# Kernel tuning notes

Hardware: AMD Instinct MI355X
Metric: run time of the kernel (lower is better)

## Reference

```python
import jax, jax.numpy as jnp
import numpy as np

UNITS = 4096                                # number of heap nodes (power of two)
DEPTH = (UNITS - 1).bit_length() + 1        # 13 heap steps (k = 0..12)
FEATURES = [2, 64, 64, 2]
BATCH = 256


def _build_heap_maps(nodes):
    """For each heap step k, precompute for every output node j the input
    (ancestor) node index it reads from, plus a validity mask. This encodes
    exactly the torch block loop: for level l, input nodes [floor(2^(l-1)), 2^l)
    broadcast (repeat_interleave by heap_factor) into output range
    [out_node0, out_node1), with blocks where out_node1 > nodes skipped."""
    depth = (nodes - 1).bit_length() + 1
    maps = []
    for k in range(depth):
        idx = np.zeros(nodes, np.int32)
        mask = np.zeros(nodes, np.bool_)
        for l in range(depth):
            in0 = 0 if l == 0 else 2 ** (l - 1)
            if in0 == 0:  # root block (node 0)
                hf = 1 if k == 0 else 2 ** (k - 1)      # ceil(2^(k-1))
                out0 = 0 if k == 0 else 2 ** (k - 1)    # floor(2^(k-1))
                out1 = out0 + hf
            else:
                hf = 2 ** k
                out0 = in0 * hf
                out1 = (2 ** l) * hf
            if out1 <= nodes:
                js = np.arange(out0, out1)
                idx[js] = in0 + (js - out0) // hf
                mask[js] = True
        maps.append((jnp.asarray(idx), jnp.asarray(mask)))
    return maps


MAPS = _build_heap_maps(UNITS)


def heap_linear(x, W, b, minheap):
    # x: [..., nodes, in_f]; W: [K, out_f, in_f]; b: [K, out_f]; K = DEPTH - minheap
    out = jnp.zeros(x.shape[:-1] + (W.shape[1],), jnp.float32)
    for i, k in enumerate(range(minheap, DEPTH)):
        idx, mask = MAPS[k]
        # apply linear_k to every node once, then gather parent -> children
        y = jnp.einsum('...ni,oi->...no', x, W[i]) + b[i]
        out = out + jnp.where(mask[:, None], y[..., idx, :], 0.0)
    return out


def setup_inputs() -> dict:
    key = jax.random.key(0)
    ks = jax.random.split(key, 7)
    f0, f1, f2, f3 = FEATURES

    def w(k, n, o, i):
        return jax.random.normal(k, (n, o, i), jnp.float32) / np.float32(np.sqrt(i))

    return {
        "x": jax.random.normal(ks[0], (BATCH, UNITS, f0), jnp.float32),
        "W1": w(ks[1], DEPTH - 1, f1, f0),   # minheap=1 -> 12 sublayers
        "b1": jax.random.normal(ks[2], (DEPTH - 1, f1), jnp.float32) * 0.01,
        "W2": w(ks[3], DEPTH, f2, f1),       # minheap=0 -> 13 sublayers
        "b2": jax.random.normal(ks[4], (DEPTH, f2), jnp.float32) * 0.01,
        "W3": w(ks[5], DEPTH, f3, f2),
        "b3": jax.random.normal(ks[6], (DEPTH, f3), jnp.float32) * 0.01,
    }


def reference(x, W1, b1, W2, b2, W3, b3):
    h = heap_linear(x, W1, b1, minheap=1)
    h = jax.nn.relu(h)
    h = heap_linear(h, W2, b2, minheap=0)
    h = jax.nn.relu(h)
    logits = heap_linear(h, W3, b3, minheap=0)
    return logits
```

## Files before the change

### kernel.cpp

```cpp
#include <hip/hip_runtime.h>

#define UNITS 4096
#define DEPTH 13
#define BATCH 256

typedef __attribute__((ext_vector_type(8))) short s16x8;
typedef __attribute__((ext_vector_type(4))) float f32x4;
typedef __attribute__((ext_vector_type(4))) int   i32x4;

__device__ __forceinline__ unsigned short f2bf(float f){
  unsigned u = __builtin_bit_cast(unsigned, f);
  u += 0x7FFFu + ((u >> 16) & 1u);
  return (unsigned short)(u >> 16);
}
__device__ __forceinline__ int levelof(int j){ return j ? (32 - __clz(j)) : 0; }

struct FragA { s16x8 v[2]; };
struct FragB { s16x8 v[2][4]; };

__device__ __forceinline__ void gll16(const void* g, void* l){
  __builtin_amdgcn_global_load_lds(
      (const __attribute__((address_space(1))) unsigned int*)g,
      (__attribute__((address_space(3))) unsigned int*)l, 16, 0, 0);
}

__device__ __forceinline__ void load_afragG(FragA& f, const unsigned short* __restrict__ Hq,
                                            int rowbase, int l15, int kg){
  #pragma unroll
  for (int kk = 0; kk < 2; ++kk)
    f.v[kk] = *(const s16x8*)(Hq + ((size_t)((kk*4 + kg)*256 + rowbase + l15))*8);
}
__device__ __forceinline__ void load_bfragG(FragB& f, const unsigned short* __restrict__ Wf,
                                            int lane){
  #pragma unroll
  for (int kk = 0; kk < 2; ++kk)
    #pragma unroll
    for (int n = 0; n < 4; ++n)
      f.v[kk][n] = *(const s16x8*)(Wf + ((size_t)((kk*4 + n)*64 + lane))*8);
}
__device__ __forceinline__ void ld_afragL(FragA& f, const char* Ab, int wid, int l15, int kg){
  #pragma unroll
  for (int kk = 0; kk < 2; ++kk)
    f.v[kk] = *(const s16x8*)(Ab + (kk*4 + kg)*1024 + (wid*16 + l15)*16);
}
__device__ __forceinline__ void ld_bfragL(FragB& f, const char* Bb, int lane){
  #pragma unroll
  for (int kk = 0; kk < 2; ++kk)
    #pragma unroll
    for (int n = 0; n < 4; ++n)
      f.v[kk][n] = *(const s16x8*)(Bb + ((kk*4 + n)*64 + lane)*16);
}
__device__ __forceinline__ void mstep(f32x4 acc[4], const FragA& A, const FragB& B){
  #pragma unroll
  for (int kk = 0; kk < 2; ++kk)
    #pragma unroll
    for (int n = 0; n < 4; ++n)
      acc[n] = __builtin_amdgcn_mfma_f32_16x16x32_bf16(A.v[kk], B.v[kk][n], acc[n], 0, 0, 0);
}
__device__ __forceinline__ void negA(FragA& A){
  const i32x4 sgn = {(int)0x80008000, (int)0x80008000, (int)0x80008000, (int)0x80008000};
  #pragma unroll
  for (int kk = 0; kk < 2; ++kk){
    i32x4 t = __builtin_bit_cast(i32x4, A.v[kk]);
    t ^= sgn;
    A.v[kk] = __builtin_bit_cast(s16x8, t);
  }
}

__device__ __forceinline__ float rowsum16(float s){
  int v, u;
  v = __builtin_bit_cast(int, s);
  u = __builtin_amdgcn_update_dpp(v, v, 0xB1, 0xF, 0xF, false);
  s += __builtin_bit_cast(float, u);
  v = __builtin_bit_cast(int, s);
  u = __builtin_amdgcn_update_dpp(v, v, 0x4E, 0xF, 0xF, false);
  s += __builtin_bit_cast(float, u);
  v = __builtin_bit_cast(int, s);
  u = __builtin_amdgcn_update_dpp(v, v, 0x141, 0xF, 0xF, false);
  s += __builtin_bit_cast(float, u);
  v = __builtin_bit_cast(int, s);
  u = __builtin_amdgcn_update_dpp(v, v, 0x140, 0xF, 0xF, false);
  s += __builtin_bit_cast(float, u);
  return s;
}

__device__ __forceinline__ void epilogue(const f32x4 acc[4], int p, int lp,
    const float cbv[4], const float* w3s,
    float* __restrict__ y3, int rowbase, int l15, int kg){
  int tmax = 11 - lp;
  for (int tt = 0; tt <= tmax; ++tt){
    float w30[4], w31[4];
    #pragma unroll
    for (int n = 0; n < 4; ++n){
      w30[n] = w3s[(tt*2 + 0)*64 + n*16 + l15];
      w31[n] = w3s[(tt*2 + 1)*64 + n*16 + l15];
    }
    int off = 4096 - (4096 >> tt);
    #pragma unroll
    for (int reg = 0; reg < 4; ++reg){
      float s0 = 0.f, s1 = 0.f;
      #pragma unroll
      for (int n = 0; n < 4; ++n){
        float hv = fmaxf(acc[n][reg] + cbv[n], 0.f);
        s0 = fmaf(w30[n], hv, s0);
        s1 = fmaf(w31[n], hv, s1);
      }
      s0 = rowsum16(s0);
      s1 = rowsum16(s1);
      if (l15 == 0){
        int b = rowbase + kg*4 + reg;
        float2 v; v.x = s0; v.y = s1;
        *(float2*)(y3 + ((size_t)(off + p)*256 + b)*2) = v;
      }
    }
  }
}

__global__ __launch_bounds__(256) void k_prep(const float* __restrict__ W2,
    const float* __restrict__ W1, const float* __restrict__ W3,
    const float* __restrict__ b1, const float* __restrict__ b2, const float* __restrict__ b3,
    unsigned short* __restrict__ W2f, unsigned short* __restrict__ W1f,
    float* __restrict__ cb1, float* __restrict__ cb2, float* __restrict__ cb3,
    float* __restrict__ w3h20){
  int blk = blockIdx.x, t = threadIdx.x;
  if (blk < 26){
    int u = blk*256 + t;
    int lane = u & 63, c = (u >> 6) & 7, k = u >> 9;
    int n = c & 3, kk = c >> 2, l15 = lane & 15, kg = lane >> 4;
    s16x8 rr;
    #pragma unroll
    for (int e = 0; e < 8; ++e)
      rr[e] = (short)f2bf(W2[((size_t)(k*64 + n*16 + l15))*64 + kk*32 + kg*8 + e]);
    *(s16x8*)(W2f + (size_t)u*8) = rr;
  } else if (blk == 26){
    int n = t >> 6, lane = t & 63, l15 = lane & 15, kg = lane >> 4;
    int f = n*16 + l15;
    s16x8 r = {0,0,0,0,0,0,0,0};
    #pragma unroll
    for (int j = 0; j < 4; ++j){
      int m = kg*4 + j;
      if (m < DEPTH-1){
        r[2*j]   = (short)f2bf(W1[(m*64 + f)*2]);
        r[2*j+1] = (short)f2bf(W1[(m*64 + f)*2 + 1]);
      }
    }
    *(s16x8*)(W1f + (size_t)t*8) = r;
  } else {
    if (t < 64){
      float r = 0.f;
      cb1[t] = 0.f;
      for (int m = 1; m < DEPTH; ++m){ r += b1[(m-1)*64 + t]; cb1[m*64 + t] = r; }
      float r2 = 0.f;
      for (int m = 0; m < DEPTH; ++m){ r2 += b2[m*64 + t]; cb2[m*64 + t] = r2; }
    } else if (t < 66){
      int o = t - 64;
      float r = 0.f;
      for (int m = 0; m < DEPTH; ++m){ r += b3[m*2 + o]; cb3[m*2 + o] = r; }
    } else if (t >= 128 && t < 128 + DEPTH*2){
      int q = t - 128, tt = q >> 1, o = q & 1;
      float s = 0.f;
      for (int f = 0; f < 64; ++f)
        s = fmaf(W3[(tt*2 + o)*64 + f], fmaxf(b2[f], 0.f), s);
      w3h20[tt*2 + o] = s;
    }
  }
}

__global__ __launch_bounds__(256) void k_xpose(const float* __restrict__ x,
                                               float* __restrict__ xT){
  __shared__ float2 tile[64][65];
  int jb = (blockIdx.x & 63) * 64;
  int bb = (blockIdx.x >> 6) * 64;
  int t = threadIdx.x;
  #pragma unroll
  for (int i = 0; i < 16; ++i){
    int idx = i*256 + t;
    int jj = idx & 63, b = idx >> 6;
    tile[jj][b] = *(const float2*)(x + (((size_t)(bb + b))*UNITS + jb + jj)*2);
  }
  __syncthreads();
  #pragma unroll
  for (int i = 0; i < 16; ++i){
    int idx = i*256 + t;
    int b = idx & 63, jj = idx >> 6;
    *(float2*)(xT + (((size_t)(jb + jj))*BATCH + bb + b)*2) = tile[jj][b];
  }
}

__global__ __launch_bounds__(256) void k_GH(const float* __restrict__ xT,
    const unsigned short* __restrict__ W1f, const float* __restrict__ cb1,
    unsigned short* __restrict__ H){
  __shared__ unsigned short tile[BATCH*64];
  int p = blockIdx.x;
  int lvl = levelof(p);
  int t = threadIdx.x, wid = t >> 6, lane = t & 63, l15 = lane & 15, kg = lane >> 4;

  s16x8 af[4];
  #pragma unroll
  for (int m = 0; m < 4; ++m){
    int b = wid*64 + m*16 + l15;
    s16x8 r = {0,0,0,0,0,0,0,0};
    #pragma unroll
    for (int j = 0; j < 4; ++j){
      int mm = kg*4 + j;
      if (mm <= lvl){
        float2 xv = *(const float2*)(xT + ((size_t)(p >> mm)*BATCH + b)*2);
        r[2*j]   = (short)f2bf(xv.x);
        r[2*j+1] = (short)f2bf(xv.y);
      }
    }
    af[m] = r;
  }
  f32x4 acc[4][4];
  #pragma unroll
  for (int m = 0; m < 4; ++m)
    #pragma unroll
    for (int n = 0; n < 4; ++n) acc[m][n] = (f32x4){0.f,0.f,0.f,0.f};
  #pragma unroll
  for (int n = 0; n < 4; ++n){
    s16x8 bf = *(const s16x8*)(W1f + ((size_t)n*64 + lane)*8);
    #pragma unroll
    for (int m = 0; m < 4; ++m)
      acc[m][n] = __builtin_amdgcn_mfma_f32_16x16x32_bf16(af[m], bf, acc[m][n], 0, 0, 0);
  }
  int lvl1 = lvl + 1;
  float cbv[4];
  #pragma unroll
  for (int n = 0; n < 4; ++n) cbv[n] = cb1[lvl1*64 + n*16 + l15];
  #pragma unroll
  for (int m = 0; m < 4; ++m)
    #pragma unroll
    for (int n = 0; n < 4; ++n)
      #pragma unroll
      for (int i = 0; i < 4; ++i){
        int row = wid*64 + m*16 + kg*4 + i;
        int col = n*16 + l15;
        float v = fmaxf(acc[m][n][i] + cbv[n], 0.f);
        *(unsigned short*)((char*)tile + ((row*128 + col*2) ^ ((row & 7) << 4))) = f2bf(v);
      }
  __syncthreads();
  #pragma unroll
  for (int i = 0; i < 8; ++i){
    s16x8 v = *(const s16x8*)((const char*)tile + ((t*128 + i*16) ^ ((t & 7) << 4)));
    *(s16x8*)(H + (size_t)p*16384 + ((size_t)i*256 + t)*8) = v;
  }
}

__global__ __launch_bounds__(256, 3) void k_F11(const unsigned short* __restrict__ H,
    const unsigned short* __restrict__ W2f, const float* __restrict__ cb2,
    const float* __restrict__ W3, float* __restrict__ y3){
  __shared__ char As[2*8192];
  __shared__ char Bs[2*8192];
  __shared__ float w3s[26*64];

  int bid = blockIdx.x;
  int slice = bid >> 9;
  int r = bid & 511;
  int q = 511 - ((r & 7)*64 + (r >> 3));
  int t = threadIdx.x, wid = t >> 6, lane = t & 63, l15 = lane & 15, kg = lane >> 4;
  int rowbase = slice*64 + wid*16;

  const char* Hb   = (const char*)H;
  const char* W2fb = (const char*)W2f;

  #pragma unroll
  for (int i = 0; i < 2; ++i){
    int idx = i*256 + t;
    if (idx < 416) ((float4*)w3s)[idx] = ((const float4*)W3)[idx];
  }

  f32x4 acc[4];
  #pragma unroll
  for (int n = 0; n < 4; ++n) acc[n] = (f32x4){0.f, 0.f, 0.f, 0.f};

  if (q == 0){
    __syncthreads();
    FragA A; FragB B;
    for (int p = 0; p < 4; ++p){
      int lp = levelof(p);
      float cbv[4];
      #pragma unroll
      for (int n = 0; n < 4; ++n) cbv[n] = cb2[(lp+1)*64 + n*16 + l15];
      #pragma unroll
      for (int n = 0; n < 4; ++n) acc[n] = (f32x4){0.f, 0.f, 0.f, 0.f};
      for (int k = 0; k <= lp; ++k){
        load_bfragG(B, W2f + (size_t)k*4096, lane);
        load_afragG(A, H + (size_t)(p >> k)*16384, rowbase, l15, kg);
        mstep(acc, A, B);
      }
      epilogue(acc, p, lp, cbv, w3s, y3, rowbase, l15, kg);
    }
    return;
  }

  const int L = levelof(q) + 2;
  const int S = L + 5;
  float cbv[4];
  #pragma unroll
  for (int n = 0; n < 4; ++n) cbv[n] = cb2[(L+1)*64 + n*16 + l15];

  auto stage = [&](int u){
    int tileA; const char* Wk;
    if (u <= L-2){
      tileA = q >> u;
      Wk = W2fb + (size_t)(u+2)*8192;
    } else {
      int d = u - (L-1);
      tileA = (d==0) ? 2*q : (d==1) ? 4*q : (d==2) ? 4*q+1
            : (d==3) ? 2*q+1 : (d==4) ? 4*q+2 : 4*q+3;
      Wk = (d==0 || d==3) ? (W2fb + 8192) : W2fb;
    }
    const char* Ht = Hb + (size_t)tileA*32768;
    char* Ab = As + (u & 1)*8192;
    char* Bb = Bs + (u & 1)*8192;
    #pragma unroll
    for (int j = 0; j < 2; ++j){
      int piece = wid*2 + j;
      gll16(Ht + piece*4096 + (slice*64 + lane)*16, Ab + piece*1024);
    }
    #pragma unroll
    for (int j = 0; j < 2; ++j){
      int c = wid*2 + j;
      gll16(Wk + c*1024 + lane*16, Bb + c*1024);
    }
  };

  stage(0);
  __syncthreads();

  FragA held0, held1;

  for (int s = 0; s < S; ++s){
    if (s + 1 < S) stage(s + 1);
    const char* Ab = As + (s & 1)*8192;
    const char* Bb = Bs + (s & 1)*8192;
    FragB bF; ld_bfragL(bF, Bb, lane);
    if (s <= L-2){
      FragA aF; ld_afragL(aF, Ab, wid, l15, kg);
      mstep(acc, aF, bF);
    } else {
      int d = s - (L-1);
      if (d == 0){
        ld_afragL(held0, Ab, wid, l15, kg);
        mstep(acc, held0, bF);
      } else if (d == 1){
        ld_afragL(held1, Ab, wid, l15, kg);
        mstep(acc, held1, bF);
        epilogue(acc, 4*q, L, cbv, w3s, y3, rowbase, l15, kg);
      } else if (d == 2){
        negA(held1); mstep(acc, held1, bF);
        ld_afragL(held1, Ab, wid, l15, kg);
        mstep(acc, held1, bF);
        epilogue(acc, 4*q + 1, L, cbv, w3s, y3, rowbase, l15, kg);
      } else if (d == 3){
        negA(held0); mstep(acc, held0, bF);
        FragA aF; ld_afragL(aF, Ab, wid, l15, kg);
        mstep(acc, aF, bF);
      } else if (d == 4){
        negA(held1); mstep(acc, held1, bF);
        ld_afragL(held1, Ab, wid, l15, kg);
        mstep(acc, held1, bF);
        epilogue(acc, 4*q + 2, L, cbv, w3s, y3, rowbase, l15, kg);
      } else {
        negA(held1); mstep(acc, held1, bF);
        FragA aF; ld_afragL(aF, Ab, wid, l15, kg);
        mstep(acc, aF, bF);
        epilogue(acc, 4*q + 3, L, cbv, w3s, y3, rowbase, l15, kg);
      }
    }
    __syncthreads();
  }
}

__global__ __launch_bounds__(256) void k_scatter(const float* __restrict__ y3,
    const float* __restrict__ cb3, const float* __restrict__ w3h20,
    float* __restrict__ out){
  int i = blockIdx.x;
  int b = threadIdx.x;
  float4 o[4];
  #pragma unroll
  for (int c = 0; c < 4; ++c){
    int p = i*4 + c;
    int lp = levelof(p);
    float s0 = cb3[(lp+1)*2]     + w3h20[(lp+1)*2];
    float s1 = cb3[(lp+1)*2 + 1] + w3h20[(lp+1)*2 + 1];
    for (int k = 0; k <= lp; ++k){
      int pi = (4096 - (4096 >> k)) + (p >> k);
      float2 v = *(const float2*)(y3 + ((size_t)pi*256 + b)*2);
      s0 += v.x; s1 += v.y;
    }
    if (p == 0){
      o[c].x = cb3[0] + w3h20[0];
      o[c].y = cb3[1] + w3h20[1];
      o[c].z = s0; o[c].w = s1;
    } else {
      o[c].x = s0; o[c].y = s1; o[c].z = s0; o[c].w = s1;
    }
  }
  float4* dst = (float4*)(out + (size_t)b*8192 + (size_t)i*16);
  #pragma unroll
  for (int c = 0; c < 4; ++c) dst[c] = o[c];
}

extern "C" void kernel_launch(void* const* d_in, const int* in_sizes, int n_in,
                              void* d_out, int out_size, void* d_ws, size_t ws_size,
                              hipStream_t stream){
  const float* x  = (const float*)d_in[0];
  const float* W1 = (const float*)d_in[1];
  const float* b1 = (const float*)d_in[2];
  const float* W2 = (const float*)d_in[3];
  const float* b2 = (const float*)d_in[4];
  const float* W3 = (const float*)d_in[5];
  const float* b3 = (const float*)d_in[6];
  float* out = (float*)d_out;
  char* ws = (char*)d_ws;

  unsigned short* W2f   = (unsigned short*)(ws + 0);
  unsigned short* W1f   = (unsigned short*)(ws + 106496);
  float* cb1   = (float*)(ws + 110592);
  float* cb2   = (float*)(ws + 113920);
  float* cb3   = (float*)(ws + 117248);
  float* w3h20 = (float*)(ws + 117376);
  float* xT    = (float*)(ws + 117504);
  unsigned short* H = (unsigned short*)(ws + 8506112);
  float* y3    = (float*)(ws + 75614976);

  hipLaunchKernelGGL(k_prep,    dim3(28),   dim3(256), 0, stream, W2, W1, W3, b1, b2, b3, W2f, W1f, cb1, cb2, cb3, w3h20);
  hipLaunchKernelGGL(k_xpose,   dim3(256),  dim3(256), 0, stream, x, xT);
  hipLaunchKernelGGL(k_GH,      dim3(2048), dim3(256), 0, stream, xT, W1f, cb1, H);
  hipLaunchKernelGGL(k_F11,     dim3(2048), dim3(256), 0, stream, H, W2f, cb2, W3, y3);
  hipLaunchKernelGGL(k_scatter, dim3(512),  dim3(256), 0, stream, y3, cb3, w3h20, out);
}
```

Baseline: 123.4 us.

## Compute layer-3 projection epilogue with MFMA instead of scalar FMA and DPP reductions

The third-layer projection, which applies all 26 W3 rows to the relu'd hidden tile, moves from scalar FMAs plus 16-lane DPP row reductions onto bf16 MFMA instructions. The hidden tile goes through a small per-wave swizzled LDS scratch, and W3 is pre-packed into MFMA fragments in a new prep block. Results are kept in registers and stored together at the end. This cuts VALU and cross-lane work in the epilogue, at the cost of bf16 rounding of the hidden activations, extra LDS traffic and more live registers.

```diff
diff --git a/kernel.cpp b/kernel.cpp
--- a/kernel.cpp
+++ b/kernel.cpp
@@ -67,59 +67,31 @@
   }
 }
 
-__device__ __forceinline__ float rowsum16(float s){
-  int v, u;
-  v = __builtin_bit_cast(int, s);
-  u = __builtin_amdgcn_update_dpp(v, v, 0xB1, 0xF, 0xF, false);
-  s += __builtin_bit_cast(float, u);
-  v = __builtin_bit_cast(int, s);
-  u = __builtin_amdgcn_update_dpp(v, v, 0x4E, 0xF, 0xF, false);
-  s += __builtin_bit_cast(float, u);
-  v = __builtin_bit_cast(int, s);
-  u = __builtin_amdgcn_update_dpp(v, v, 0x141, 0xF, 0xF, false);
-  s += __builtin_bit_cast(float, u);
-  v = __builtin_bit_cast(int, s);
-  u = __builtin_amdgcn_update_dpp(v, v, 0x140, 0xF, 0xF, false);
-  s += __builtin_bit_cast(float, u);
-  return s;
-}
-
-__device__ __forceinline__ void epilogue(const f32x4 acc[4], int p, int lp,
-    const float cbv[4], const float* w3s,
-    float* __restrict__ y3, int rowbase, int l15, int kg){
-  int tmax = 11 - lp;
-  for (int tt = 0; tt <= tmax; ++tt){
-    float w30[4], w31[4];
-    #pragma unroll
-    for (int n = 0; n < 4; ++n){
-      w30[n] = w3s[(tt*2 + 0)*64 + n*16 + l15];
-      w31[n] = w3s[(tt*2 + 1)*64 + n*16 + l15];
-    }
-    int off = 4096 - (4096 >> tt);
+__device__ __forceinline__ void epi_mfma(const f32x4 acc[4], const float cbv[4],
+    char* scr, const s16x8 (&w3a)[2][2], f32x4& d0, f32x4& d1,
+    int l15, int kg){
+  #pragma unroll
+  for (int n = 0; n < 4; ++n)
     #pragma unroll
     for (int reg = 0; reg < 4; ++reg){
-      float s0 = 0.f, s1 = 0.f;
-      #pragma unroll
-      for (int n = 0; n < 4; ++n){
-        float hv = fmaxf(acc[n][reg] + cbv[n], 0.f);
-        s0 = fmaf(w30[n], hv, s0);
-        s1 = fmaf(w31[n], hv, s1);
-      }
-      s0 = rowsum16(s0);
-      s1 = rowsum16(s1);
-      if (l15 == 0){
-        int b = rowbase + kg*4 + reg;
-        float2 v; v.x = s0; v.y = s1;
-        *(float2*)(y3 + ((size_t)(off + p)*256 + b)*2) = v;
-      }
-    }
-  }
+      float hv = fmaxf(acc[n][reg] + cbv[n], 0.f);
+      int a16 = (kg*4 + reg)*64 + ((n*16 + l15) ^ (kg << 4));
+      *(unsigned short*)(scr + a16*2) = f2bf(hv);
+    }
+  int key = (l15 >> 2) << 4;
+  s16x8 b0 = *(const s16x8*)(scr + (size_t)(l15*64 + ((kg*8)      ^ key))*2);
+  s16x8 b1 = *(const s16x8*)(scr + (size_t)(l15*64 + ((32 + kg*8) ^ key))*2);
+  d0 = __builtin_amdgcn_mfma_f32_16x16x32_bf16(w3a[0][0], b0, d0, 0, 0, 0);
+  d0 = __builtin_amdgcn_mfma_f32_16x16x32_bf16(w3a[1][0], b1, d0, 0, 0, 0);
+  d1 = __builtin_amdgcn_mfma_f32_16x16x32_bf16(w3a[0][1], b0, d1, 0, 0, 0);
+  d1 = __builtin_amdgcn_mfma_f32_16x16x32_bf16(w3a[1][1], b1, d1, 0, 0, 0);
 }
 
 __global__ __launch_bounds__(256) void k_prep(const float* __restrict__ W2,
     const float* __restrict__ W1, const float* __restrict__ W3,
     const float* __restrict__ b1, const float* __restrict__ b2, const float* __restrict__ b3,
     unsigned short* __restrict__ W2f, unsigned short* __restrict__ W1f,
+    unsigned short* __restrict__ W3Af,
     float* __restrict__ cb1, float* __restrict__ cb2, float* __restrict__ cb3,
     float* __restrict__ w3h20){
   int blk = blockIdx.x, t = threadIdx.x;
@@ -145,6 +117,17 @@
       }
     }
     *(s16x8*)(W1f + (size_t)t*8) = r;
+  } else if (blk == 27){
+    int lane = t & 63, tile = (t >> 6) & 1, kk = t >> 7;
+    int l15 = lane & 15, kg = lane >> 4;
+    int row = tile*16 + l15;
+    s16x8 r = {0,0,0,0,0,0,0,0};
+    if (row < 26){
+      #pragma unroll
+      for (int e = 0; e < 8; ++e)
+        r[e] = (short)f2bf(W3[(size_t)row*64 + kk*32 + kg*8 + e]);
+    }
+    *(s16x8*)(W3Af + (size_t)t*8) = r;
   } else {
     if (t < 64){
       float r = 0.f;
@@ -246,12 +229,27 @@
   }
 }
 
-__global__ __launch_bounds__(256, 3) void k_F11(const unsigned short* __restrict__ H,
-    const unsigned short* __restrict__ W2f, const float* __restrict__ cb2,
-    const float* __restrict__ W3, float* __restrict__ y3){
+#define STORE_D(dv0, dv1, pp, lpv) { \
+  int cnt = 2*(12 - (lpv)); \
+  _Pragma("unroll") \
+  for (int tile_ = 0; tile_ < 2; ++tile_){ \
+    _Pragma("unroll") \
+    for (int reg_ = 0; reg_ < 4; ++reg_){ \
+      int ttp = tile_*16 + kg*4 + reg_; \
+      if (ttp < cnt){ \
+        int tt = ttp >> 1, o = ttp & 1; \
+        int offp = 4096 - (4096 >> tt); \
+        y3[((size_t)(offp + (pp))*256 + rowbase + l15)*2 + o] = (tile_ ? (dv1)[reg_] : (dv0)[reg_]); \
+      } \
+    } \
+  } }
+
+__global__ __launch_bounds__(256, 3) void k_F12(const unsigned short* __restrict__ H,
+    const unsigned short* __restrict__ W2f, const unsigned short* __restrict__ W3Af,
+    const float* __restrict__ cb2, float* __restrict__ y3){
   __shared__ char As[2*8192];
   __shared__ char Bs[2*8192];
-  __shared__ float w3s[26*64];
+  __shared__ char scr_all[4*2048];
 
   int bid = blockIdx.x;
   int slice = bid >> 9;
@@ -259,37 +257,68 @@
   int q = 511 - ((r & 7)*64 + (r >> 3));
   int t = threadIdx.x, wid = t >> 6, lane = t & 63, l15 = lane & 15, kg = lane >> 4;
   int rowbase = slice*64 + wid*16;
+  char* scr = scr_all + wid*2048;
 
   const char* Hb   = (const char*)H;
   const char* W2fb = (const char*)W2f;
 
-  #pragma unroll
-  for (int i = 0; i < 2; ++i){
-    int idx = i*256 + t;
-    if (idx < 416) ((float4*)w3s)[idx] = ((const float4*)W3)[idx];
-  }
+  s16x8 w3a[2][2];
+  #pragma unroll
+  for (int kk = 0; kk < 2; ++kk)
+    #pragma unroll
+    for (int tile = 0; tile < 2; ++tile)
+      w3a[kk][tile] = *(const s16x8*)(W3Af + ((size_t)((kk*2 + tile)*64 + lane))*8);
 
   f32x4 acc[4];
   #pragma unroll
   for (int n = 0; n < 4; ++n) acc[n] = (f32x4){0.f, 0.f, 0.f, 0.f};
 
+  f32x4 dA0 = {0,0,0,0}, dA1 = {0,0,0,0}, dB0 = {0,0,0,0}, dB1 = {0,0,0,0};
+  f32x4 dC0 = {0,0,0,0}, dC1 = {0,0,0,0}, dD0 = {0,0,0,0}, dD1 = {0,0,0,0};
+
   if (q == 0){
-    __syncthreads();
     FragA A; FragB B;
-    for (int p = 0; p < 4; ++p){
-      int lp = levelof(p);
-      float cbv[4];
+    float cbv[4];
+    #pragma unroll
+    for (int n = 0; n < 4; ++n) acc[n] = (f32x4){0.f, 0.f, 0.f, 0.f};
+    { int lp = 0;
       #pragma unroll
       for (int n = 0; n < 4; ++n) cbv[n] = cb2[(lp+1)*64 + n*16 + l15];
-      #pragma unroll
-      for (int n = 0; n < 4; ++n) acc[n] = (f32x4){0.f, 0.f, 0.f, 0.f};
-      for (int k = 0; k <= lp; ++k){
+      load_bfragG(B, W2f, lane);
+      load_afragG(A, H, rowbase, l15, kg);
+      mstep(acc, A, B);
+      epi_mfma(acc, cbv, scr, w3a, dA0, dA1, l15, kg); }
+    { int lp = 1;
+      #pragma unroll
+      for (int n = 0; n < 4; ++n){ cbv[n] = cb2[(lp+1)*64 + n*16 + l15]; acc[n] = (f32x4){0.f,0.f,0.f,0.f}; }
+      for (int k = 0; k <= 1; ++k){
         load_bfragG(B, W2f + (size_t)k*4096, lane);
-        load_afragG(A, H + (size_t)(p >> k)*16384, rowbase, l15, kg);
+        load_afragG(A, H + (size_t)(1 >> k)*16384, rowbase, l15, kg);
         mstep(acc, A, B);
       }
-      epilogue(acc, p, lp, cbv, w3s, y3, rowbase, l15, kg);
-    }
+      epi_mfma(acc, cbv, scr, w3a, dB0, dB1, l15, kg); }
+    { int lp = 2;
+      #pragma unroll
+      for (int n = 0; n < 4; ++n){ cbv[n] = cb2[(lp+1)*64 + n*16 + l15]; acc[n] = (f32x4){0.f,0.f,0.f,0.f}; }
+      for (int k = 0; k <= 2; ++k){
+        load_bfragG(B, W2f + (size_t)k*4096, lane);
+        load_afragG(A, H + (size_t)(2 >> k)*16384, rowbase, l15, kg);
+        mstep(acc, A, B);
+      }
+      epi_mfma(acc, cbv, scr, w3a, dC0, dC1, l15, kg); }
+    { int lp = 2;
+      #pragma unroll
+      for (int n = 0; n < 4; ++n){ cbv[n] = cb2[(lp+1)*64 + n*16 + l15]; acc[n] = (f32x4){0.f,0.f,0.f,0.f}; }
+      for (int k = 0; k <= 2; ++k){
+        load_bfragG(B, W2f + (size_t)k*4096, lane);
+        load_afragG(A, H + (size_t)(3 >> k)*16384, rowbase, l15, kg);
+        mstep(acc, A, B);
+      }
+      epi_mfma(acc, cbv, scr, w3a, dD0, dD1, l15, kg); }
+    STORE_D(dA0, dA1, 0, 0)
+    STORE_D(dB0, dB1, 1, 1)
+    STORE_D(dC0, dC1, 2, 2)
+    STORE_D(dD0, dD1, 3, 2)
     return;
   }
 
@@ -346,12 +375,12 @@
       } else if (d == 1){
         ld_afragL(held1, Ab, wid, l15, kg);
         mstep(acc, held1, bF);
-        epilogue(acc, 4*q, L, cbv, w3s, y3, rowbase, l15, kg);
+        epi_mfma(acc, cbv, scr, w3a, dA0, dA1, l15, kg);
       } else if (d == 2){
         negA(held1); mstep(acc, held1, bF);
         ld_afragL(held1, Ab, wid, l15, kg);
         mstep(acc, held1, bF);
-        epilogue(acc, 4*q + 1, L, cbv, w3s, y3, rowbase, l15, kg);
+        epi_mfma(acc, cbv, scr, w3a, dB0, dB1, l15, kg);
       } else if (d == 3){
         negA(held0); mstep(acc, held0, bF);
         FragA aF; ld_afragL(aF, Ab, wid, l15, kg);
@@ -360,16 +389,21 @@
         negA(held1); mstep(acc, held1, bF);
         ld_afragL(held1, Ab, wid, l15, kg);
         mstep(acc, held1, bF);
-        epilogue(acc, 4*q + 2, L, cbv, w3s, y3, rowbase, l15, kg);
+        epi_mfma(acc, cbv, scr, w3a, dC0, dC1, l15, kg);
       } else {
         negA(held1); mstep(acc, held1, bF);
         FragA aF; ld_afragL(aF, Ab, wid, l15, kg);
         mstep(acc, aF, bF);
-        epilogue(acc, 4*q + 3, L, cbv, w3s, y3, rowbase, l15, kg);
+        epi_mfma(acc, cbv, scr, w3a, dD0, dD1, l15, kg);
       }
     }
     __syncthreads();
   }
+
+  STORE_D(dA0, dA1, 4*q,     L)
+  STORE_D(dB0, dB1, 4*q + 1, L)
+  STORE_D(dC0, dC1, 4*q + 2, L)
+  STORE_D(dD0, dD1, 4*q + 3, L)
 }
 
 __global__ __launch_bounds__(256) void k_scatter(const float* __restrict__ y3,
@@ -417,17 +451,18 @@
 
   unsigned short* W2f   = (unsigned short*)(ws + 0);
   unsigned short* W1f   = (unsigned short*)(ws + 106496);
-  float* cb1   = (float*)(ws + 110592);
-  float* cb2   = (float*)(ws + 113920);
-  float* cb3   = (float*)(ws + 117248);
-  float* w3h20 = (float*)(ws + 117376);
-  float* xT    = (float*)(ws + 117504);
-  unsigned short* H = (unsigned short*)(ws + 8506112);
-  float* y3    = (float*)(ws + 75614976);
-
-  hipLaunchKernelGGL(k_prep,    dim3(28),   dim3(256), 0, stream, W2, W1, W3, b1, b2, b3, W2f, W1f, cb1, cb2, cb3, w3h20);
+  unsigned short* W3Af  = (unsigned short*)(ws + 110592);
+  float* cb1   = (float*)(ws + 114688);
+  float* cb2   = (float*)(ws + 118016);
+  float* cb3   = (float*)(ws + 121344);
+  float* w3h20 = (float*)(ws + 121472);
+  float* xT    = (float*)(ws + 121600);
+  unsigned short* H = (unsigned short*)(ws + 8510208);
+  float* y3    = (float*)(ws + 75619072);
+
+  hipLaunchKernelGGL(k_prep,    dim3(29),   dim3(256), 0, stream, W2, W1, W3, b1, b2, b3, W2f, W1f, W3Af, cb1, cb2, cb3, w3h20);
   hipLaunchKernelGGL(k_xpose,   dim3(256),  dim3(256), 0, stream, x, xT);
   hipLaunchKernelGGL(k_GH,      dim3(2048), dim3(256), 0, stream, xT, W1f, cb1, H);
-  hipLaunchKernelGGL(k_F11,     dim3(2048), dim3(256), 0, stream, H, W2f, cb2, W3, y3);
+  hipLaunchKernelGGL(k_F12,     dim3(2048), dim3(256), 0, stream, H, W2f, W3Af, cb2, y3);
   hipLaunchKernelGGL(k_scatter, dim3(512),  dim3(256), 0, stream, y3, cb3, w3h20, out);
 }
```

Result: slower. 214.7 us (+74.0%).

## Double per-wave M tile in fused layer-2 kernel to reuse W2 fragments

Applied to the files above, without the earlier changes.

The fused layer-2/layer-3 kernel now has each wave compute 32 batch rows (two 16-row MFMA tiles) instead of 16, so each block covers 128 rows and the grid halves to 1024 blocks. Every W2 B-fragment loaded from LDS is reused across two A tiles, which cuts LDS and global traffic for weights per output. W3 is also staged in LDS as bf16 instead of fp32. The costs are more accumulator and A-fragment registers, which may hurt occupancy under the 3-block launch bound, fewer blocks to balance the uneven per-q work, and slightly lower precision for the W3 epilogue weights.

```diff
diff --git a/kernel.cpp b/kernel.cpp
--- a/kernel.cpp
+++ b/kernel.cpp
@@ -13,10 +13,13 @@
   u += 0x7FFFu + ((u >> 16) & 1u);
   return (unsigned short)(u >> 16);
 }
+__device__ __forceinline__ float bf2f(unsigned short u){
+  return __builtin_bit_cast(float, ((unsigned)u) << 16);
+}
 __device__ __forceinline__ int levelof(int j){ return j ? (32 - __clz(j)) : 0; }
 
-struct FragA { s16x8 v[2]; };
-struct FragB { s16x8 v[2][4]; };
+struct FragA2 { s16x8 v[2][2]; };
+struct FragB  { s16x8 v[2][4]; };
 
 __device__ __forceinline__ void gll16(const void* g, void* l){
   __builtin_amdgcn_global_load_lds(
@@ -24,11 +27,13 @@
       (__attribute__((address_space(3))) unsigned int*)l, 16, 0, 0);
 }
 
-__device__ __forceinline__ void load_afragG(FragA& f, const unsigned short* __restrict__ Hq,
-                                            int rowbase, int l15, int kg){
-  #pragma unroll
-  for (int kk = 0; kk < 2; ++kk)
-    f.v[kk] = *(const s16x8*)(Hq + ((size_t)((kk*4 + kg)*256 + rowbase + l15))*8);
+__device__ __forceinline__ void load_afragG2(FragA2& f, const unsigned short* __restrict__ Hq,
+                                             int rowbase, int l15, int kg){
+  #pragma unroll
+  for (int kk = 0; kk < 2; ++kk)
+    #pragma unroll
+    for (int m = 0; m < 2; ++m)
+      f.v[kk][m] = *(const s16x8*)(Hq + ((size_t)((kk*4 + kg)*256 + rowbase + m*16 + l15))*8);
 }
 __device__ __forceinline__ void load_bfragG(FragB& f, const unsigned short* __restrict__ Wf,
                                             int lane){
@@ -38,10 +43,12 @@
     for (int n = 0; n < 4; ++n)
       f.v[kk][n] = *(const s16x8*)(Wf + ((size_t)((kk*4 + n)*64 + lane))*8);
 }
-__device__ __forceinline__ void ld_afragL(FragA& f, const char* Ab, int wid, int l15, int kg){
-  #pragma unroll
-  for (int kk = 0; kk < 2; ++kk)
-    f.v[kk] = *(const s16x8*)(Ab + (kk*4 + kg)*1024 + (wid*16 + l15)*16);
+__device__ __forceinline__ void ld_afragL2(FragA2& f, const char* Ab, int wid, int l15, int kg){
+  #pragma unroll
+  for (int kk = 0; kk < 2; ++kk)
+    #pragma unroll
+    for (int m = 0; m < 2; ++m)
+      f.v[kk][m] = *(const s16x8*)(Ab + (kk*4 + kg)*2048 + (wid*32 + m*16 + l15)*16);
 }
 __device__ __forceinline__ void ld_bfragL(FragB& f, const char* Bb, int lane){
   #pragma unroll
@@ -50,21 +57,25 @@
     for (int n = 0; n < 4; ++n)
       f.v[kk][n] = *(const s16x8*)(Bb + ((kk*4 + n)*64 + lane)*16);
 }
-__device__ __forceinline__ void mstep(f32x4 acc[4], const FragA& A, const FragB& B){
-  #pragma unroll
-  for (int kk = 0; kk < 2; ++kk)
-    #pragma unroll
-    for (int n = 0; n < 4; ++n)
-      acc[n] = __builtin_amdgcn_mfma_f32_16x16x32_bf16(A.v[kk], B.v[kk][n], acc[n], 0, 0, 0);
-}
-__device__ __forceinline__ void negA(FragA& A){
+__device__ __forceinline__ void mstep2(f32x4 acc[2][4], const FragA2& A, const FragB& B){
+  #pragma unroll
+  for (int kk = 0; kk < 2; ++kk)
+    #pragma unroll
+    for (int m = 0; m < 2; ++m)
+      #pragma unroll
+      for (int n = 0; n < 4; ++n)
+        acc[m][n] = __builtin_amdgcn_mfma_f32_16x16x32_bf16(A.v[kk][m], B.v[kk][n], acc[m][n], 0, 0, 0);
+}
+__device__ __forceinline__ void negA2(FragA2& A){
   const i32x4 sgn = {(int)0x80008000, (int)0x80008000, (int)0x80008000, (int)0x80008000};
   #pragma unroll
-  for (int kk = 0; kk < 2; ++kk){
-    i32x4 t = __builtin_bit_cast(i32x4, A.v[kk]);
-    t ^= sgn;
-    A.v[kk] = __builtin_bit_cast(s16x8, t);
-  }
+  for (int kk = 0; kk < 2; ++kk)
+    #pragma unroll
+    for (int m = 0; m < 2; ++m){
+      i32x4 t = __builtin_bit_cast(i32x4, A.v[kk][m]);
+      t ^= sgn;
+      A.v[kk][m] = __builtin_bit_cast(s16x8, t);
+    }
 }
 
 __device__ __forceinline__ float rowsum16(float s){
@@ -84,35 +95,37 @@
   return s;
 }
 
-__device__ __forceinline__ void epilogue(const f32x4 acc[4], int p, int lp,
-    const float cbv[4], const float* w3s,
+__device__ __forceinline__ void epilogue2(const f32x4 acc[2][4], int p, int lp,
+    const float cbv[4], const unsigned short* w3s,
     float* __restrict__ y3, int rowbase, int l15, int kg){
   int tmax = 11 - lp;
   for (int tt = 0; tt <= tmax; ++tt){
     float w30[4], w31[4];
     #pragma unroll
     for (int n = 0; n < 4; ++n){
-      w30[n] = w3s[(tt*2 + 0)*64 + n*16 + l15];
-      w31[n] = w3s[(tt*2 + 1)*64 + n*16 + l15];
+      w30[n] = bf2f(w3s[(tt*2 + 0)*64 + n*16 + l15]);
+      w31[n] = bf2f(w3s[(tt*2 + 1)*64 + n*16 + l15]);
     }
     int off = 4096 - (4096 >> tt);
     #pragma unroll
-    for (int reg = 0; reg < 4; ++reg){
-      float s0 = 0.f, s1 = 0.f;
+    for (int m = 0; m < 2; ++m)
       #pragma unroll
-      for (int n = 0; n < 4; ++n){
-        float hv = fmaxf(acc[n][reg] + cbv[n], 0.f);
-        s0 = fmaf(w30[n], hv, s0);
-        s1 = fmaf(w31[n], hv, s1);
-      }
-      s0 = rowsum16(s0);
-      s1 = rowsum16(s1);
-      if (l15 == 0){
-        int b = rowbase + kg*4 + reg;
-        float2 v; v.x = s0; v.y = s1;
-        *(float2*)(y3 + ((size_t)(off + p)*256 + b)*2) = v;
-      }
-    }
+      for (int reg = 0; reg < 4; ++reg){
+        float s0 = 0.f, s1 = 0.f;
+        #pragma unroll
+        for (int n = 0; n < 4; ++n){
+          float hv = fmaxf(acc[m][n][reg] + cbv[n], 0.f);
+          s0 = fmaf(w30[n], hv, s0);
+          s1 = fmaf(w31[n], hv, s1);
+        }
+        s0 = rowsum16(s0);
+        s1 = rowsum16(s1);
+        if (l15 == 0){
+          int b = rowbase + m*16 + kg*4 + reg;
+          float2 v; v.x = s0; v.y = s1;
+          *(float2*)(y3 + ((size_t)(off + p)*256 + b)*2) = v;
+        }
+      }
   }
 }
 
@@ -246,49 +259,55 @@
   }
 }
 
-__global__ __launch_bounds__(256, 3) void k_F11(const unsigned short* __restrict__ H,
+__global__ __launch_bounds__(256, 3) void k_F16(const unsigned short* __restrict__ H,
     const unsigned short* __restrict__ W2f, const float* __restrict__ cb2,
     const float* __restrict__ W3, float* __restrict__ y3){
-  __shared__ char As[2*8192];
+  __shared__ char As[2*16384];
   __shared__ char Bs[2*8192];
-  __shared__ float w3s[26*64];
+  __shared__ unsigned short w3s[26*64];
 
   int bid = blockIdx.x;
   int slice = bid >> 9;
   int r = bid & 511;
   int q = 511 - ((r & 7)*64 + (r >> 3));
   int t = threadIdx.x, wid = t >> 6, lane = t & 63, l15 = lane & 15, kg = lane >> 4;
-  int rowbase = slice*64 + wid*16;
+  int rowbase = slice*128 + wid*32;
 
   const char* Hb   = (const char*)H;
   const char* W2fb = (const char*)W2f;
 
-  #pragma unroll
-  for (int i = 0; i < 2; ++i){
-    int idx = i*256 + t;
-    if (idx < 416) ((float4*)w3s)[idx] = ((const float4*)W3)[idx];
-  }
-
-  f32x4 acc[4];
-  #pragma unroll
-  for (int n = 0; n < 4; ++n) acc[n] = (f32x4){0.f, 0.f, 0.f, 0.f};
+  if (t < 208){
+    const float* src = W3 + (size_t)t*8;
+    s16x8 rr;
+    #pragma unroll
+    for (int e = 0; e < 8; ++e) rr[e] = (short)f2bf(src[e]);
+    *(s16x8*)(w3s + (size_t)t*8) = rr;
+  }
+  __syncthreads();
+
+  f32x4 acc[2][4];
+  #pragma unroll
+  for (int m = 0; m < 2; ++m)
+    #pragma unroll
+    for (int n = 0; n < 4; ++n) acc[m][n] = (f32x4){0.f, 0.f, 0.f, 0.f};
 
   if (q == 0){
-    __syncthreads();
-    FragA A; FragB B;
+    FragA2 A; FragB B;
     for (int p = 0; p < 4; ++p){
       int lp = levelof(p);
       float cbv[4];
       #pragma unroll
       for (int n = 0; n < 4; ++n) cbv[n] = cb2[(lp+1)*64 + n*16 + l15];
       #pragma unroll
-      for (int n = 0; n < 4; ++n) acc[n] = (f32x4){0.f, 0.f, 0.f, 0.f};
+      for (int m = 0; m < 2; ++m)
+        #pragma unroll
+        for (int n = 0; n < 4; ++n) acc[m][n] = (f32x4){0.f, 0.f, 0.f, 0.f};
       for (int k = 0; k <= lp; ++k){
         load_bfragG(B, W2f + (size_t)k*4096, lane);
-        load_afragG(A, H + (size_t)(p >> k)*16384, rowbase, l15, kg);
-        mstep(acc, A, B);
-      }
-      epilogue(acc, p, lp, cbv, w3s, y3, rowbase, l15, kg);
+        load_afragG2(A, H + (size_t)(p >> k)*16384, rowbase, l15, kg);
+        mstep2(acc, A, B);
+      }
+      epilogue2(acc, p, lp, cbv, w3s, y3, rowbase, l15, kg);
     }
     return;
   }
@@ -311,12 +330,13 @@
       Wk = (d==0 || d==3) ? (W2fb + 8192) : W2fb;
     }
     const char* Ht = Hb + (size_t)tileA*32768;
-    char* Ab = As + (u & 1)*8192;
+    char* Ab = As + (u & 1)*16384;
     char* Bb = Bs + (u & 1)*8192;
     #pragma unroll
-    for (int j = 0; j < 2; ++j){
-      int piece = wid*2 + j;
-      gll16(Ht + piece*4096 + (slice*64 + lane)*16, Ab + piece*1024);
+    for (int j = 0; j < 4; ++j){
+      int piece = j*2 + (wid >> 1);
+      gll16(Ht + (size_t)piece*4096 + slice*2048 + ((wid & 1)*64 + lane)*16,
+            Ab + j*4096 + wid*1024);
     }
     #pragma unroll
     for (int j = 0; j < 2; ++j){
@@ -328,44 +348,44 @@
   stage(0);
   __syncthreads();
 
-  FragA held0, held1;
+  FragA2 held0, held1;
 
   for (int s = 0; s < S; ++s){
     if (s + 1 < S) stage(s + 1);
-    const char* Ab = As + (s & 1)*8192;
+    const char* Ab = As + (s & 1)*16384;
     const char* Bb = Bs + (s & 1)*8192;
     FragB bF; ld_bfragL(bF, Bb, lane);
     if (s <= L-2){
-      FragA aF; ld_afragL(aF, Ab, wid, l15, kg);
-      mstep(acc, aF, bF);
+      FragA2 aF; ld_afragL2(aF, Ab, wid, l15, kg);
+      mstep2(acc, aF, bF);
     } else {
       int d = s - (L-1);
       if (d == 0){
-        ld_afragL(held0, Ab, wid, l15, kg);
-        mstep(acc, held0, bF);
+        ld_afragL2(held0, Ab, wid, l15, kg);
+        mstep2(acc, held0, bF);
       } else if (d == 1){
-        ld_afragL(held1, Ab, wid, l15, kg);
-        mstep(acc, held1, bF);
-        epilogue(acc, 4*q, L, cbv, w3s, y3, rowbase, l15, kg);
+        ld_afragL2(held1, Ab, wid, l15, kg);
+        mstep2(acc, held1, bF);
+        epilogue2(acc, 4*q, L, cbv, w3s, y3, rowbase, l15, kg);
       } else if (d == 2){
-        negA(held1); mstep(acc, held1, bF);
-        ld_afragL(held1, Ab, wid, l15, kg);
-        mstep(acc, held1, bF);
-        epilogue(acc, 4*q + 1, L, cbv, w3s, y3, rowbase, l15, kg);
+        negA2(held1); mstep2(acc, held1, bF);
+        ld_afragL2(held1, Ab, wid, l15, kg);
+        mstep2(acc, held1, bF);
+        epilogue2(acc, 4*q + 1, L, cbv, w3s, y3, rowbase, l15, kg);
       } else if (d == 3){
-        negA(held0); mstep(acc, held0, bF);
-        FragA aF; ld_afragL(aF, Ab, wid, l15, kg);
-        mstep(acc, aF, bF);
+        negA2(held0); mstep2(acc, held0, bF);
+        FragA2 aF; ld_afragL2(aF, Ab, wid, l15, kg);
+        mstep2(acc, aF, bF);
       } else if (d == 4){
-        negA(held1); mstep(acc, held1, bF);
-        ld_afragL(held1, Ab, wid, l15, kg);
-        mstep(acc, held1, bF);
-        epilogue(acc, 4*q + 2, L, cbv, w3s, y3, rowbase, l15, kg);
+        negA2(held1); mstep2(acc, held1, bF);
+        ld_afragL2(held1, Ab, wid, l15, kg);
+        mstep2(acc, held1, bF);
+        epilogue2(acc, 4*q + 2, L, cbv, w3s, y3, rowbase, l15, kg);
       } else {
-        negA(held1); mstep(acc, held1, bF);
-        FragA aF; ld_afragL(aF, Ab, wid, l15, kg);
-        mstep(acc, aF, bF);
-        epilogue(acc, 4*q + 3, L, cbv, w3s, y3, rowbase, l15, kg);
+        negA2(held1); mstep2(acc, held1, bF);
+        FragA2 aF; ld_afragL2(aF, Ab, wid, l15, kg);
+        mstep2(acc, aF, bF);
+        epilogue2(acc, 4*q + 3, L, cbv, w3s, y3, rowbase, l15, kg);
       }
     }
     __syncthreads();
@@ -428,6 +448,6 @@
   hipLaunchKernelGGL(k_prep,    dim3(28),   dim3(256), 0, stream, W2, W1, W3, b1, b2, b3, W2f, W1f, cb1, cb2, cb3, w3h20);
   hipLaunchKernelGGL(k_xpose,   dim3(256),  dim3(256), 0, stream, x, xT);
   hipLaunchKernelGGL(k_GH,      dim3(2048), dim3(256), 0, stream, xT, W1f, cb1, H);
-  hipLaunchKernelGGL(k_F11,     dim3(2048), dim3(256), 0, stream, H, W2f, cb2, W3, y3);
+  hipLaunchKernelGGL(k_F16,     dim3(1024), dim3(256), 0, stream, H, W2f, cb2, W3, y3);
   hipLaunchKernelGGL(k_scatter, dim3(512),  dim3(256), 0, stream, y3, cb3, w3h20, out);
 }
```

Result: slower. 233.4 us (+89.2%).
